# Performance work log

Hardware: AMD Instinct MI355X
Metric: run time of the kernel (lower is better)

The kernel has to match this reference:

```python
import jax, jax.numpy as jnp
import numpy as np

NUM_HEADS = 16
DEPTH = 0


def rotate_half(x):
    x1, x2 = jnp.split(x, 2, axis=-1)
    return jnp.concatenate((-x2, x1), axis=-1)


def rotary_tables(seq_len, rot_dim, dtype):
    # RotaryEmbedding(dim=rot_dim): inv_freq over even indices of rot_dim
    inv_freq = 1.0 / (10000.0 ** (jnp.arange(0, rot_dim, 2, dtype=jnp.float32) / rot_dim))
    freqs = jnp.arange(seq_len, dtype=jnp.float32)[:, None] * inv_freq[None, :]  # [N, rot_dim/2]
    emb = jnp.concatenate((freqs, freqs), axis=-1)  # [N, rot_dim]
    return emb.astype(dtype), jnp.cos(emb).astype(dtype), jnp.sin(emb).astype(dtype)


def setup_inputs() -> dict:
    key = jax.random.key(0)
    ks = jax.random.split(key, 7)
    B, N, C = 1, 2048, 1024
    hd = C // NUM_HEADS
    std_qkv = (1.0 / C) ** 0.5
    std_proj = (1.0 / (2 * C)) ** 0.5
    return {
        "x": jax.random.normal(ks[0], (B, N, C), dtype=jnp.float32),
        "W_qkv": jax.random.normal(ks[1], (6 * C, C), dtype=jnp.float32) * std_qkv,
        "W_proj": jax.random.normal(ks[2], (C, 2 * C), dtype=jnp.float32) * std_proj,
        "lambda_q1": jax.random.normal(ks[3], (hd,), dtype=jnp.float32) * 0.1,
        "lambda_q2": jax.random.normal(ks[4], (hd,), dtype=jnp.float32) * 0.1,
        "lambda_k1": jax.random.normal(ks[5], (hd,), dtype=jnp.float32) * 0.1,
        "lambda_k2": jax.random.normal(ks[6], (hd,), dtype=jnp.float32) * 0.1,
    }


def reference(x, W_qkv, W_proj, lambda_q1, lambda_q2, lambda_k1, lambda_k2):
    B, N, C = x.shape
    H = NUM_HEADS
    hd = C // H
    scale = hd ** -0.5
    lambda_init = 0.8 - 0.6 * np.exp(-0.3 * DEPTH)

    qkv = jnp.einsum('bnc,dc->bnd', x, W_qkv)               # [B,N,6C]
    qkv = qkv.reshape(B, N, 6, H, hd).transpose(2, 0, 3, 1, 4)  # [6,B,H,N,hd]
    q = jnp.concatenate((qkv[0], qkv[1]), axis=-1)          # [B,H,N,2hd]
    k = jnp.concatenate((qkv[2], qkv[3]), axis=-1)
    v = jnp.concatenate((qkv[4], qkv[5]), axis=-1)

    _, cos, sin = rotary_tables(N, 2 * hd, x.dtype)          # [N,2hd]
    q = q * cos + rotate_half(q) * sin
    k = k * cos + rotate_half(k) * sin

    q1, q2 = jnp.split(q, 2, axis=-1)                        # [B,H,N,hd] each
    k1, k2 = jnp.split(k, 2, axis=-1)

    attn1 = jnp.einsum('bhid,bhjd->bhij', q1, k1) * scale
    attn2 = jnp.einsum('bhid,bhjd->bhij', q2, k2) * scale

    lam1 = jnp.exp(jnp.sum(lambda_q1 * lambda_k1))
    lam2 = jnp.exp(jnp.sum(lambda_q2 * lambda_k2))
    lam = (lam1 - lam2 + lambda_init).astype(x.dtype)

    probs = jax.nn.softmax(attn1, axis=-1) - lam * jax.nn.softmax(attn2, axis=-1)
    out = jnp.einsum('bhij,bhjd->bhid', probs, v)            # [B,H,N,2hd]
    out = out.transpose(0, 2, 1, 3).reshape(B, N, 2 * C)
    out = jnp.einsum('bnd,cd->bnc', out, W_proj)             # [B,N,C]
    return out
```

## Files before the change

### kernel.cpp

```cpp
#include <hip/hip_runtime.h>

using bf16_t = __bf16;
typedef __bf16 bf16x4 __attribute__((ext_vector_type(4)));
typedef __bf16 bf16x8 __attribute__((ext_vector_type(8)));
typedef float floatx4 __attribute__((ext_vector_type(4)));

#define MFMA_BF16(a, b, c) __builtin_amdgcn_mfma_f32_16x16x32_bf16((a), (b), (c), 0, 0, 0)

__device__ __forceinline__ void async_ld16(bf16_t* lds_dst, const bf16_t* g_src) {
    __builtin_amdgcn_global_load_lds(
        (const __attribute__((address_space(1))) void*)g_src,
        (__attribute__((address_space(3))) void*)lds_dst, 16, 0, 0);
}

__global__ __launch_bounds__(256) void cast_all(const float* __restrict__ x,
                                                const float* __restrict__ Wqkv,
                                                const float* __restrict__ Wproj,
                                                const float* __restrict__ lq1,
                                                const float* __restrict__ lq2,
                                                const float* __restrict__ lk1,
                                                const float* __restrict__ lk2,
                                                bf16_t* __restrict__ xb,
                                                bf16_t* __restrict__ Wqkvb,
                                                bf16_t* __restrict__ Wprojb,
                                                float* __restrict__ lamp) {
    const int b = blockIdx.x;
    if (b == 5120) {
        int l = threadIdx.x;
        if (l < 64) {
            float p1 = lq1[l] * lk1[l];
            float p2 = lq2[l] * lk2[l];
            #pragma unroll
            for (int d = 1; d < 64; d <<= 1) {
                p1 += __shfl_xor(p1, d);
                p2 += __shfl_xor(p2, d);
            }
            if (l == 0) *lamp = expf(p1) - expf(p2) + 0.2f;
        }
        return;
    }
    const float* src;
    bf16_t* dst;
    size_t i;
    if (b < 1024)      { src = x;     dst = xb;     i = (size_t)b * 256 + threadIdx.x; }
    else if (b < 4096) { src = Wqkv;  dst = Wqkvb;  i = (size_t)(b - 1024) * 256 + threadIdx.x; }
    else               { src = Wproj; dst = Wprojb; i = (size_t)(b - 4096) * 256 + threadIdx.x; }
    const floatx4 a = *(const floatx4*)(src + i * 8);
    const floatx4 c = *(const floatx4*)(src + i * 8 + 4);
    bf16x8 r;
    r[0] = (bf16_t)a[0]; r[1] = (bf16_t)a[1]; r[2] = (bf16_t)a[2]; r[3] = (bf16_t)a[3];
    r[4] = (bf16_t)c[0]; r[5] = (bf16_t)c[1]; r[6] = (bf16_t)c[2]; r[7] = (bf16_t)c[3];
    *(bf16x8*)(dst + i * 8) = r;
}

__global__ __launch_bounds__(512, 4) void gemm_qkv8(const bf16_t* __restrict__ A,
                                                    const bf16_t* __restrict__ B,
                                                    bf16_t* __restrict__ Qb,
                                                    bf16_t* __restrict__ Kb,
                                                    bf16_t* __restrict__ Vt) {
    constexpr int K = 1024;
    __shared__ __align__(16) bf16_t As[2][128 * 32];
    __shared__ __align__(16) bf16_t Bs[2][128 * 32];
    const int t = threadIdx.x;
    const int lane = t & 63, wave = t >> 6;
    const int q4 = lane >> 4, m16 = lane & 15;
    const int mblk = blockIdx.y * 128, nblk = blockIdx.x * 128;
    const int wr = wave >> 2, wc = wave & 3;

    auto stage = [&](int buf, int k0) {
        async_ld16(&As[buf][t * 8], &A[(size_t)(mblk + (t >> 2)) * K + k0 + (t & 3) * 8]);
        async_ld16(&Bs[buf][t * 8], &B[(size_t)(nblk + (t >> 2)) * K + k0 + (t & 3) * 8]);
    };

    floatx4 acc[4][2] = {};
    stage(0, 0);

    for (int it = 0; it < 32; ++it) {
        const int cur = it & 1;
        __syncthreads();
        if (it + 1 < 32) stage(cur ^ 1, (it + 1) * 32);

        bf16x8 a[4], b[2];
        #pragma unroll
        for (int i = 0; i < 4; ++i)
            a[i] = *(const bf16x8*)&As[cur][(wr * 64 + i * 16 + m16) * 32 + q4 * 8];
        #pragma unroll
        for (int j = 0; j < 2; ++j)
            b[j] = *(const bf16x8*)&Bs[cur][(wc * 32 + j * 16 + m16) * 32 + q4 * 8];
        __builtin_amdgcn_s_setprio(1);
        #pragma unroll
        for (int i = 0; i < 4; ++i)
            #pragma unroll
            for (int j = 0; j < 2; ++j)
                acc[i][j] = MFMA_BF16(a[i], b[j], acc[i][j]);
        __builtin_amdgcn_s_setprio(0);
    }

    #pragma unroll
    for (int i = 0; i < 4; ++i)
        #pragma unroll
        for (int j = 0; j < 2; ++j) {
            int n = nblk + wc * 32 + j * 16 + m16;
            int mbase = mblk + wr * 64 + i * 16 + q4 * 4;
            int comp = n >> 10, h = (n >> 6) & 15, e = n & 63;
            if (comp < 2) {
                #pragma unroll
                for (int r = 0; r < 4; ++r)
                    Qb[(size_t)((comp * 16 + h) * 2048 + mbase + r) * 64 + e] =
                        (bf16_t)acc[i][j][r];
            } else if (comp < 4) {
                #pragma unroll
                for (int r = 0; r < 4; ++r)
                    Kb[(size_t)(((comp - 2) * 16 + h) * 2048 + mbase + r) * 64 + e] =
                        (bf16_t)acc[i][j][r];
            } else {
                bf16x4 pv;
                #pragma unroll
                for (int r = 0; r < 4; ++r) pv[r] = (bf16_t)acc[i][j][r];
                *(bf16x4*)&Vt[(size_t)(h * 128 + (comp - 4) * 64 + e) * 2048 + mbase] = pv;
            }
        }
}

template <int BM, int BN, int BK, bool QKV_EPI, typename TC>
__global__ __launch_bounds__(256) void gemm_bt(const bf16_t* __restrict__ A,
                                               const bf16_t* __restrict__ B,
                                               TC* __restrict__ C,
                                               bf16_t* __restrict__ Qb,
                                               bf16_t* __restrict__ Kb,
                                               bf16_t* __restrict__ Vt,
                                               int M, int N, int K) {
    constexpr int KC = BK / 32;
    constexpr int CH = BK / 8;
    constexpr int AR = BM * BK / 2048;
    constexpr int BR = BN * BK / 2048;
    __shared__ __align__(16) bf16_t As[2][BM * BK];
    __shared__ __align__(16) bf16_t Bs[2][BN * BK];
    const int t = threadIdx.x;
    const int lane = t & 63, wave = t >> 6;
    const int q4 = lane >> 4, m16 = lane & 15;
    const int mblk = blockIdx.y * BM, nblk = blockIdx.x * BN;
    const int wr = wave >> 1, wc = wave & 1;
    constexpr int WM = BM / 2, WN = BN / 2;
    constexpr int NI = WM / 16, NJ = WN / 16;

    auto stage = [&](int buf, int k0) {
        #pragma unroll
        for (int rr = 0; rr < AR; ++rr) {
            int f = rr * 256 + t;
            async_ld16(&As[buf][f * 8], &A[(size_t)(mblk + f / CH) * K + k0 + (f % CH) * 8]);
        }
        #pragma unroll
        for (int rr = 0; rr < BR; ++rr) {
            int f = rr * 256 + t;
            async_ld16(&Bs[buf][f * 8], &B[(size_t)(nblk + f / CH) * K + k0 + (f % CH) * 8]);
        }
    };

    floatx4 acc[NI][NJ] = {};
    stage(0, 0);

    const int NTK = K / BK;
    for (int it = 0; it < NTK; ++it) {
        const int cur = it & 1;
        __syncthreads();
        if (it + 1 < NTK) stage(cur ^ 1, (it + 1) * BK);

        bf16x8 a[NI][KC], b[NJ][KC];
        #pragma unroll
        for (int i = 0; i < NI; ++i)
            #pragma unroll
            for (int kk = 0; kk < KC; ++kk)
                a[i][kk] = *(const bf16x8*)&As[cur][(wr * WM + i * 16 + m16) * BK + kk * 32 + q4 * 8];
        #pragma unroll
        for (int j = 0; j < NJ; ++j)
            #pragma unroll
            for (int kk = 0; kk < KC; ++kk)
                b[j][kk] = *(const bf16x8*)&Bs[cur][(wc * WN + j * 16 + m16) * BK + kk * 32 + q4 * 8];
        __builtin_amdgcn_s_setprio(1);
        #pragma unroll
        for (int i = 0; i < NI; ++i)
            #pragma unroll
            for (int j = 0; j < NJ; ++j)
                #pragma unroll
                for (int kk = 0; kk < KC; ++kk)
                    acc[i][j] = MFMA_BF16(a[i][kk], b[j][kk], acc[i][j]);
        __builtin_amdgcn_s_setprio(0);
    }

    #pragma unroll
    for (int i = 0; i < NI; ++i)
        #pragma unroll
        for (int j = 0; j < NJ; ++j) {
            int n = nblk + wc * WN + j * 16 + m16;
            int mbase = mblk + wr * WM + i * 16 + q4 * 4;
            if constexpr (QKV_EPI) {
                int comp = n >> 10, h = (n >> 6) & 15, e = n & 63;
                if (comp < 2) {
                    #pragma unroll
                    for (int r = 0; r < 4; ++r)
                        Qb[(size_t)((comp * 16 + h) * 2048 + mbase + r) * 64 + e] =
                            (bf16_t)acc[i][j][r];
                } else if (comp < 4) {
                    #pragma unroll
                    for (int r = 0; r < 4; ++r)
                        Kb[(size_t)(((comp - 2) * 16 + h) * 2048 + mbase + r) * 64 + e] =
                            (bf16_t)acc[i][j][r];
                } else {
                    bf16x4 pv;
                    #pragma unroll
                    for (int r = 0; r < 4; ++r) pv[r] = (bf16_t)acc[i][j][r];
                    *(bf16x4*)&Vt[(size_t)(h * 128 + (comp - 4) * 64 + e) * 2048 + mbase] = pv;
                }
            } else {
                #pragma unroll
                for (int r = 0; r < 4; ++r)
                    C[(size_t)(mbase + r) * N + n] = (TC)acc[i][j][r];
            }
        }
}

__global__ __launch_bounds__(256) void rotary_inplace(bf16_t* __restrict__ Qb,
                                                      bf16_t* __restrict__ Kb) {
    int t = blockIdx.x * 256 + threadIdx.x;
    int e = t & 63, n = t >> 6;
    float invf = exp2f(-(float)e * (13.287712379549449f / 64.0f));
    float ang = (float)n * invf;
    float s, c;
    sincosf(ang, &s, &c);
    #pragma unroll 4
    for (int h = 0; h < 16; ++h) {
        int off = (h * 2048 + n) * 64 + e;
        float q1 = (float)Qb[off], q2 = (float)Qb[off + 2097152];
        Qb[off]           = (bf16_t)(q1 * c - q2 * s);
        Qb[off + 2097152] = (bf16_t)(q2 * c + q1 * s);
        float k1 = (float)Kb[off], k2 = (float)Kb[off + 2097152];
        Kb[off]           = (bf16_t)(k1 * c - k2 * s);
        Kb[off + 2097152] = (bf16_t)(k2 * c + k1 * s);
    }
}

__global__ __launch_bounds__(512, 4) void flash_diff(const bf16_t* __restrict__ Qb,
                                                     const bf16_t* __restrict__ Kb,
                                                     const bf16_t* __restrict__ Vt,
                                                     const float* __restrict__ lamp,
                                                     bf16_t* __restrict__ Ao) {
    constexpr int N = 2048, BN = 64, NT = N / BN;
    __shared__ __align__(16) bf16_t smem[40960];
    bf16_t* Pf = smem + 32768;
    const int t = threadIdx.x, lane = t & 63, w = t >> 6;
    const int comp = w >> 2, w4 = w & 3;
    const int q4 = lane >> 4, m16 = lane & 15;
    const int Lb = blockIdx.x;
    const int virt = (Lb & 7) * 64 + (Lb >> 3);
    const int h = virt >> 5, qt = virt & 31;
    const float lam = *lamp;
    const float cexp = 0.125f * 1.4426950408889634f;

    bf16x8 qf[2];
    const int qrow = qt * 64 + w4 * 16 + m16;
    #pragma unroll
    for (int kc = 0; kc < 2; ++kc)
        qf[kc] = *(const bf16x8*)&Qb[(size_t)((comp * 16 + h) * 2048 + qrow) * 64 + kc * 32 + q4 * 8];

    bf16x8 ones;
    #pragma unroll
    for (int j = 0; j < 8; ++j) ones[j] = (bf16_t)1.0f;

    floatx4 O[8] = {};
    floatx4 sm = {};

    auto stage = [&](bf16_t* Kd, bf16_t* Vd, int k0) {
        #pragma unroll
        for (int rr = 0; rr < 4; ++rr) {
            int idx = w * 4 + rr;
            if (idx < 16) {
                int i = idx >> 3, s = (idx >> 1) & 3, half = idx & 1;
                async_ld16(&Kd[idx * 512],
                           &Kb[(size_t)((i * 16 + h) * 2048 + k0 + 16 * s + m16) * 64 + half * 32 + q4 * 8]);
            } else {
                int v = idx - 16, tt = v >> 1, half = v & 1;
                async_ld16(&Vd[v * 512],
                           &Vt[(size_t)(h * 128 + tt * 16 + m16) * 2048 + k0 + half * 32 + q4 * 8]);
            }
        }
    };

    stage(smem, smem + 8192, 0);

    for (int it = 0; it < NT; ++it) {
        const int cur = it & 1;
        bf16_t* Kf = smem + cur * 16384;
        bf16_t* Vf = Kf + 8192;
        __syncthreads();
        if (it + 1 < NT) {
            bf16_t* Kn = smem + (cur ^ 1) * 16384;
            stage(Kn, Kn + 8192, (it + 1) * BN);
        }

        bf16_t* pw = &Pf[w * 1024];
        __builtin_amdgcn_s_setprio(1);
        #pragma unroll
        for (int s = 0; s < 4; ++s) {
            floatx4 sacc = {};
            const bf16x8 kf0 = *(const bf16x8*)&Kf[((comp * 4 + s) * 2 + 0) * 512 + lane * 8];
            const bf16x8 kf1 = *(const bf16x8*)&Kf[((comp * 4 + s) * 2 + 1) * 512 + lane * 8];
            sacc = MFMA_BF16(qf[0], kf0, sacc);
            sacc = MFMA_BF16(qf[1], kf1, sacc);
            __builtin_amdgcn_s_setprio(0);
            const int half = s >> 1, quad = (2 * s + (m16 >> 3)) & 3, jj = m16 & 7;
            #pragma unroll
            for (int r = 0; r < 4; ++r) {
                int u = quad * 16 + q4 * 4 + r;
                pw[half * 512 + (u ^ quad) * 8 + jj] = (bf16_t)exp2f(sacc[r] * cexp);
            }
            __builtin_amdgcn_s_setprio(1);
        }
        __builtin_amdgcn_s_setprio(0);

        bf16x8 pf[2];
        const int ur = lane ^ q4;
        pf[0] = *(const bf16x8*)&pw[0 * 512 + ur * 8];
        pf[1] = *(const bf16x8*)&pw[1 * 512 + ur * 8];
        sm = MFMA_BF16(pf[0], ones, sm);
        sm = MFMA_BF16(pf[1], ones, sm);
        __builtin_amdgcn_s_setprio(1);
        #pragma unroll
        for (int tt = 0; tt < 8; ++tt) {
            const bf16x8 vf0 = *(const bf16x8*)&Vf[(tt * 2 + 0) * 512 + lane * 8];
            const bf16x8 vf1 = *(const bf16x8*)&Vf[(tt * 2 + 1) * 512 + lane * 8];
            O[tt] = MFMA_BF16(pf[0], vf0, O[tt]);
            O[tt] = MFMA_BF16(pf[1], vf1, O[tt]);
        }
        __builtin_amdgcn_s_setprio(0);
    }

    float inv[4];
    #pragma unroll
    for (int r = 0; r < 4; ++r) inv[r] = 1.0f / sm[r];

    float* Ff = (float*)smem;
    __syncthreads();
    if (comp == 1) {
        #pragma unroll
        for (int tt = 0; tt < 8; ++tt) {
            floatx4 val;
            #pragma unroll
            for (int r = 0; r < 4; ++r) val[r] = lam * O[tt][r] * inv[r];
            *(floatx4*)&Ff[((w4 * 128 + tt * 16 + m16) << 4) + q4 * 4] = val;
        }
    }
    __syncthreads();
    if (comp == 0) {
        const int orow = qt * 64 + w4 * 16 + q4 * 4;
        #pragma unroll
        for (int tt = 0; tt < 8; ++tt) {
            const floatx4 v1 = *(const floatx4*)&Ff[((w4 * 128 + tt * 16 + m16) << 4) + q4 * 4];
            #pragma unroll
            for (int r = 0; r < 4; ++r) {
                float val = O[tt][r] * inv[r] - v1[r];
                Ao[(size_t)(orow + r) * 2048 + h * 128 + tt * 16 + m16] = (bf16_t)val;
            }
        }
    }
}

extern "C" void kernel_launch(void* const* d_in, const int* in_sizes, int n_in,
                              void* d_out, int out_size, void* d_ws, size_t ws_size,
                              hipStream_t stream) {
    const float* x     = (const float*)d_in[0];
    const float* Wqkv  = (const float*)d_in[1];
    const float* Wproj = (const float*)d_in[2];
    const float* lq1   = (const float*)d_in[3];
    const float* lq2   = (const float*)d_in[4];
    const float* lk1   = (const float*)d_in[5];
    const float* lk2   = (const float*)d_in[6];
    float* out = (float*)d_out;

    char* ws = (char*)d_ws;
    bf16_t* xb     = (bf16_t*)(ws);
    bf16_t* Ao     = (bf16_t*)(ws);
    bf16_t* Wqkvb  = (bf16_t*)(ws + 4194304);
    bf16_t* Wprojb = (bf16_t*)(ws + 16777216);
    bf16_t* Qb     = (bf16_t*)(ws + 20971520);
    bf16_t* Kb     = (bf16_t*)(ws + 29360128);
    bf16_t* Vt     = (bf16_t*)(ws + 37748736);
    float*  lamp   = (float*)(ws + 46137344);

    cast_all<<<5121, 256, 0, stream>>>(x, Wqkv, Wproj, lq1, lq2, lk1, lk2,
                                       xb, Wqkvb, Wprojb, lamp);
    gemm_qkv8<<<dim3(48, 16), 512, 0, stream>>>(xb, Wqkvb, Qb, Kb, Vt);
    rotary_inplace<<<(2048 * 64) / 256, 256, 0, stream>>>(Qb, Kb);
    flash_diff<<<512, 512, 0, stream>>>(Qb, Kb, Vt, lamp, Ao);
    gemm_bt<64, 64, 64, false, float><<<dim3(16, 32), 256, 0, stream>>>(
        Ao, Wprojb, out, (bf16_t*)nullptr, (bf16_t*)nullptr, (bf16_t*)nullptr,
        2048, 1024, 2048);
}
```

Before: 238.4 us.

## Fuse rotary embedding into QKV GEMM epilogue with paired-column B tiles

Removes the separate rotary_inplace kernel by computing sin/cos rotation in the QKV GEMM epilogue. To make this possible, each block's B tile gathers the two rotary halves of one head (rows h*64 and 1024+h*64), so the paired values sit in the same thread's accumulators. The GEMM moves from 512 to 256 threads with a 4x4 accumulator tile per wave. This saves a read-modify-write pass over Q and K plus a launch, at the cost of per-element sincosf in the epilogue and higher register pressure.

```diff
diff --git a/kernel.cpp b/kernel.cpp
--- a/kernel.cpp
+++ b/kernel.cpp
@@ -53,26 +53,38 @@
     *(bf16x8*)(dst + i * 8) = r;
 }
 
-__global__ __launch_bounds__(512, 4) void gemm_qkv8(const bf16_t* __restrict__ A,
+__global__ __launch_bounds__(256) void gemm_qkv_rot(const bf16_t* __restrict__ A,
                                                     const bf16_t* __restrict__ B,
                                                     bf16_t* __restrict__ Qb,
                                                     bf16_t* __restrict__ Kb,
                                                     bf16_t* __restrict__ Vt) {
-    constexpr int K = 1024;
-    __shared__ __align__(16) bf16_t As[2][128 * 32];
-    __shared__ __align__(16) bf16_t Bs[2][128 * 32];
+    constexpr int K = 1024, BM = 128, BK = 32;
+    __shared__ __align__(16) bf16_t As[2][BM * BK];
+    __shared__ __align__(16) bf16_t Bs[2][BM * BK];
     const int t = threadIdx.x;
     const int lane = t & 63, wave = t >> 6;
     const int q4 = lane >> 4, m16 = lane & 15;
-    const int mblk = blockIdx.y * 128, nblk = blockIdx.x * 128;
-    const int wr = wave >> 2, wc = wave & 3;
+    const int mblk = blockIdx.y * BM;
+    const int p = blockIdx.x >> 4, hh = blockIdx.x & 15;
+    const int pbase = p * 2048 + hh * 64;
+    const int wr = wave >> 1, wc = wave & 1;
 
     auto stage = [&](int buf, int k0) {
-        async_ld16(&As[buf][t * 8], &A[(size_t)(mblk + (t >> 2)) * K + k0 + (t & 3) * 8]);
-        async_ld16(&Bs[buf][t * 8], &B[(size_t)(nblk + (t >> 2)) * K + k0 + (t & 3) * 8]);
+        #pragma unroll
+        for (int rr = 0; rr < 2; ++rr) {
+            int f = rr * 256 + t;
+            async_ld16(&As[buf][f * 8], &A[(size_t)(mblk + (f >> 2)) * K + k0 + (f & 3) * 8]);
+        }
+        #pragma unroll
+        for (int rr = 0; rr < 2; ++rr) {
+            int f = rr * 256 + t;
+            int rp = f >> 2, jt = rp >> 4;
+            int Brow = pbase + (jt & 1) * 1024 + ((jt >> 1) * 16) + (rp & 15);
+            async_ld16(&Bs[buf][f * 8], &B[(size_t)Brow * K + k0 + (f & 3) * 8]);
+        }
     };
 
-    floatx4 acc[4][2] = {};
+    floatx4 acc[4][4] = {};
     stage(0, 0);
 
     for (int it = 0; it < 32; ++it) {
@@ -80,55 +92,62 @@
         __syncthreads();
         if (it + 1 < 32) stage(cur ^ 1, (it + 1) * 32);
 
-        bf16x8 a[4], b[2];
+        bf16x8 a[4], b[4];
         #pragma unroll
         for (int i = 0; i < 4; ++i)
             a[i] = *(const bf16x8*)&As[cur][(wr * 64 + i * 16 + m16) * 32 + q4 * 8];
         #pragma unroll
-        for (int j = 0; j < 2; ++j)
-            b[j] = *(const bf16x8*)&Bs[cur][(wc * 32 + j * 16 + m16) * 32 + q4 * 8];
+        for (int j = 0; j < 4; ++j)
+            b[j] = *(const bf16x8*)&Bs[cur][(wc * 64 + j * 16 + m16) * 32 + q4 * 8];
         __builtin_amdgcn_s_setprio(1);
         #pragma unroll
         for (int i = 0; i < 4; ++i)
             #pragma unroll
-            for (int j = 0; j < 2; ++j)
+            for (int j = 0; j < 4; ++j)
                 acc[i][j] = MFMA_BF16(a[i], b[j], acc[i][j]);
         __builtin_amdgcn_s_setprio(0);
     }
 
-    #pragma unroll
-    for (int i = 0; i < 4; ++i)
-        #pragma unroll
-        for (int j = 0; j < 2; ++j) {
-            int n = nblk + wc * 32 + j * 16 + m16;
+    if (p < 2) {
+        bf16_t* dst = (p == 0) ? Qb : Kb;
+        #pragma unroll
+        for (int i = 0; i < 4; ++i) {
             int mbase = mblk + wr * 64 + i * 16 + q4 * 4;
-            int comp = n >> 10, h = (n >> 6) & 15, e = n & 63;
-            if (comp < 2) {
+            #pragma unroll
+            for (int jp = 0; jp < 2; ++jp) {
+                int e = (wc * 2 + jp) * 16 + m16;
+                float invf = exp2f(-(float)e * (13.287712379549449f / 64.0f));
                 #pragma unroll
-                for (int r = 0; r < 4; ++r)
-                    Qb[(size_t)((comp * 16 + h) * 2048 + mbase + r) * 64 + e] =
-                        (bf16_t)acc[i][j][r];
-            } else if (comp < 4) {
-                #pragma unroll
-                for (int r = 0; r < 4; ++r)
-                    Kb[(size_t)(((comp - 2) * 16 + h) * 2048 + mbase + r) * 64 + e] =
-                        (bf16_t)acc[i][j][r];
-            } else {
+                for (int r = 0; r < 4; ++r) {
+                    int m = mbase + r;
+                    float sn, cs;
+                    sincosf((float)m * invf, &sn, &cs);
+                    float v1 = acc[i][2 * jp][r], v2 = acc[i][2 * jp + 1][r];
+                    dst[(size_t)(hh * 2048 + m) * 64 + e]        = (bf16_t)(v1 * cs - v2 * sn);
+                    dst[(size_t)((16 + hh) * 2048 + m) * 64 + e] = (bf16_t)(v2 * cs + v1 * sn);
+                }
+            }
+        }
+    } else {
+        #pragma unroll
+        for (int i = 0; i < 4; ++i) {
+            int mbase = mblk + wr * 64 + i * 16 + q4 * 4;
+            #pragma unroll
+            for (int j = 0; j < 4; ++j) {
+                int inst = j & 1, e = (wc * 2 + (j >> 1)) * 16 + m16;
                 bf16x4 pv;
                 #pragma unroll
                 for (int r = 0; r < 4; ++r) pv[r] = (bf16_t)acc[i][j][r];
-                *(bf16x4*)&Vt[(size_t)(h * 128 + (comp - 4) * 64 + e) * 2048 + mbase] = pv;
-            }
-        }
-}
-
-template <int BM, int BN, int BK, bool QKV_EPI, typename TC>
+                *(bf16x4*)&Vt[(size_t)(hh * 128 + inst * 64 + e) * 2048 + mbase] = pv;
+            }
+        }
+    }
+}
+
+template <int BM, int BN, int BK>
 __global__ __launch_bounds__(256) void gemm_bt(const bf16_t* __restrict__ A,
                                                const bf16_t* __restrict__ B,
-                                               TC* __restrict__ C,
-                                               bf16_t* __restrict__ Qb,
-                                               bf16_t* __restrict__ Kb,
-                                               bf16_t* __restrict__ Vt,
+                                               float* __restrict__ C,
                                                int M, int N, int K) {
     constexpr int KC = BK / 32;
     constexpr int CH = BK / 8;
@@ -194,50 +213,10 @@
         for (int j = 0; j < NJ; ++j) {
             int n = nblk + wc * WN + j * 16 + m16;
             int mbase = mblk + wr * WM + i * 16 + q4 * 4;
-            if constexpr (QKV_EPI) {
-                int comp = n >> 10, h = (n >> 6) & 15, e = n & 63;
-                if (comp < 2) {
-                    #pragma unroll
-                    for (int r = 0; r < 4; ++r)
-                        Qb[(size_t)((comp * 16 + h) * 2048 + mbase + r) * 64 + e] =
-                            (bf16_t)acc[i][j][r];
-                } else if (comp < 4) {
-                    #pragma unroll
-                    for (int r = 0; r < 4; ++r)
-                        Kb[(size_t)(((comp - 2) * 16 + h) * 2048 + mbase + r) * 64 + e] =
-                            (bf16_t)acc[i][j][r];
-                } else {
-                    bf16x4 pv;
-                    #pragma unroll
-                    for (int r = 0; r < 4; ++r) pv[r] = (bf16_t)acc[i][j][r];
-                    *(bf16x4*)&Vt[(size_t)(h * 128 + (comp - 4) * 64 + e) * 2048 + mbase] = pv;
-                }
-            } else {
-                #pragma unroll
-                for (int r = 0; r < 4; ++r)
-                    C[(size_t)(mbase + r) * N + n] = (TC)acc[i][j][r];
-            }
-        }
-}
-
-__global__ __launch_bounds__(256) void rotary_inplace(bf16_t* __restrict__ Qb,
-                                                      bf16_t* __restrict__ Kb) {
-    int t = blockIdx.x * 256 + threadIdx.x;
-    int e = t & 63, n = t >> 6;
-    float invf = exp2f(-(float)e * (13.287712379549449f / 64.0f));
-    float ang = (float)n * invf;
-    float s, c;
-    sincosf(ang, &s, &c);
-    #pragma unroll 4
-    for (int h = 0; h < 16; ++h) {
-        int off = (h * 2048 + n) * 64 + e;
-        float q1 = (float)Qb[off], q2 = (float)Qb[off + 2097152];
-        Qb[off]           = (bf16_t)(q1 * c - q2 * s);
-        Qb[off + 2097152] = (bf16_t)(q2 * c + q1 * s);
-        float k1 = (float)Kb[off], k2 = (float)Kb[off + 2097152];
-        Kb[off]           = (bf16_t)(k1 * c - k2 * s);
-        Kb[off + 2097152] = (bf16_t)(k2 * c + k1 * s);
-    }
+            #pragma unroll
+            for (int r = 0; r < 4; ++r)
+                C[(size_t)(mbase + r) * N + n] = acc[i][j][r];
+        }
 }
 
 __global__ __launch_bounds__(512, 4) void flash_diff(const bf16_t* __restrict__ Qb,
@@ -389,10 +368,8 @@
 
     cast_all<<<5121, 256, 0, stream>>>(x, Wqkv, Wproj, lq1, lq2, lk1, lk2,
                                        xb, Wqkvb, Wprojb, lamp);
-    gemm_qkv8<<<dim3(48, 16), 512, 0, stream>>>(xb, Wqkvb, Qb, Kb, Vt);
-    rotary_inplace<<<(2048 * 64) / 256, 256, 0, stream>>>(Qb, Kb);
+    gemm_qkv_rot<<<dim3(48, 16), 256, 0, stream>>>(xb, Wqkvb, Qb, Kb, Vt);
     flash_diff<<<512, 512, 0, stream>>>(Qb, Kb, Vt, lamp, Ao);
-    gemm_bt<64, 64, 64, false, float><<<dim3(16, 32), 256, 0, stream>>>(
-        Ao, Wprojb, out, (bf16_t*)nullptr, (bf16_t*)nullptr, (bf16_t*)nullptr,
-        2048, 1024, 2048);
-}
+    gemm_bt<64, 64, 64><<<dim3(16, 32), 256, 0, stream>>>(
+        Ao, Wprojb, out, 2048, 1024, 2048);
+}
```

Result: faster. 233.0 us (-2.3%).
